# Performance work log

Measured on AMD Instinct MI355X. Metric: run time of the kernel, lower is better.

## Reference

```python
import jax, jax.numpy as jnp
import numpy as np


def _jac_det(u):
    # u: [B, 3, D, H, W] displacement field in [-1, 1]-normalized coords
    B, C, D, H, W = u.shape
    scale = jnp.array([(D - 1) / 2.0, (H - 1) / 2.0, (W - 1) / 2.0], dtype=u.dtype)
    phi = u * scale[None, :, None, None, None]
    px, py, pz = phi[:, 0], phi[:, 1], phi[:, 2]  # each [B, D, H, W]
    # torch.gradient == numpy.gradient: central differences interior, one-sided edges
    gx = lambda a: jnp.gradient(a, axis=-3)
    gy = lambda a: jnp.gradient(a, axis=-2)
    gz = lambda a: jnp.gradient(a, axis=-1)
    dxx = gx(px) + 1.0
    dxy = gy(px)
    dxz = gz(px)
    dyx = gx(py)
    dyy = gy(py) + 1.0
    dyz = gz(py)
    dzx = gx(pz)
    dzy = gy(pz)
    dzz = gz(pz) + 1.0
    det = (dxx * (dyy * dzz - dyz * dzy)
           + dxy * (dyz * dzx - dyx * dzz)
           + dxz * (dyx * dzy - dyy * dzx))
    return det


def setup_inputs() -> dict:
    key = jax.random.key(0)
    displacement_field = jax.random.normal(key, (2, 3, 160, 192, 160), dtype=jnp.float32) * 0.05
    return {"displacement_field": displacement_field}


def reference(displacement_field):
    det = _jac_det(displacement_field)
    # loss = mean(relu(-det))
    return jnp.mean(jax.nn.relu(-det))
```

## Files before the change

kernel.cpp:

```cpp
#include <hip/hip_runtime.h>

#define Dd 160
#define Hh 192
#define Ww 160
#define HW (Hh * Ww)
#define DHW ((size_t)Dd * HW)
#define NVOX_D 9830400.0

#define TH 8
#define TD 10
#define QROW (Ww / 4)
#define TPB (QROW * TH)
#define NHT (Hh / TH)
#define NDS (Dd / TD)
#define GRID1 (2 * NHT * NDS)
#define BLK2 256

__device__ __forceinline__ float4 ld4(const float* p) {
    return *reinterpret_cast<const float4*>(p);
}

__device__ __forceinline__ float4 wgrad(float4 cc, float lft, float rgt, int w0) {
    float4 g;
    g.x = (w0 == 0)      ? (cc.y - cc.x) : 0.5f * (cc.y - lft);
    g.y = 0.5f * (cc.z - cc.x);
    g.z = 0.5f * (cc.w - cc.y);
    g.w = (w0 + 4 == Ww) ? (cc.w - cc.z) : 0.5f * (rgt - cc.z);
    return g;
}

__device__ __forceinline__ float relu_negdet(
    float gd0, float gh0, float gw0,
    float gd1, float gh1, float gw1,
    float gd2, float gh2, float gw2)
{
    const float sx = 79.5f;
    const float sy = 95.5f;
    const float sz = 79.5f;
    float dxx = fmaf(sx, gd0, 1.0f);
    float dxy = sx * gh0;
    float dxz = sx * gw0;
    float dyx = sy * gd1;
    float dyy = fmaf(sy, gh1, 1.0f);
    float dyz = sy * gw1;
    float dzx = sz * gd2;
    float dzy = sz * gh2;
    float dzz = fmaf(sz, gw2, 1.0f);
    float det = dxx * (dyy * dzz - dyz * dzy)
              + dxy * (dyz * dzx - dyx * dzz)
              + dxz * (dyx * dzy - dyy * dzx);
    return fmaxf(-det, 0.0f);
}

__global__ __launch_bounds__(TPB) void jac_partial(const float* __restrict__ u,
                                                   float* __restrict__ part)
{
    const int gid = blockIdx.x;
    const int ds  = gid % NDS;
    const int ht  = (gid / NDS) % NHT;
    const int b   = gid / (NDS * NHT);

    const int tid = threadIdx.x;
    const int wq  = tid % QROW;
    const int hh  = tid / QROW;
    const int h   = ht * TH + hh;
    const int w0  = wq * 4;

    const int hm = (h > 0)      ? h - 1 : 0;
    const int hp = (h < Hh - 1) ? h + 1 : Hh - 1;
    const float hinv = 1.0f / (float)(hp - hm);
    const int offm = (hm - h) * Ww;
    const int offp = (hp - h) * Ww;

    const int d0 = ds * TD;

    const float* pcA = u + (size_t)(b * 3 + 0) * DHW + (size_t)h * Ww + w0;
    const float* pcB = pcA + DHW;
    const float* pcC = pcA + 2 * DHW;

    float4 a0, a1, b0, b1, c0, c1;
    {
        const size_t om = (size_t)((d0 > 0) ? d0 - 1 : 0) * HW;
        const size_t oc = (size_t)d0 * HW;
        a0 = ld4(pcA + om);  a1 = ld4(pcA + oc);
        b0 = ld4(pcB + om);  b1 = ld4(pcB + oc);
        c0 = ld4(pcC + om);  c1 = ld4(pcC + oc);
    }

    float acc = 0.0f;

    #pragma unroll 2
    for (int d = d0; d < d0 + TD; ++d) {
        const int dp = (d < Dd - 1) ? d + 1 : Dd - 1;
        const float dinv = (d > 0 && d < Dd - 1) ? 0.5f : 1.0f;
        const size_t od  = (size_t)d  * HW;
        const size_t odp = (size_t)dp * HW;

        float4 a2 = ld4(pcA + odp);
        float4 b2 = ld4(pcB + odp);
        float4 c2 = ld4(pcC + odp);

        const float* pdA = pcA + od;
        const float* pdB = pcB + od;
        const float* pdC = pcC + od;

        float4 rAm = ld4(pdA + offm), rAp = ld4(pdA + offp);
        float4 rBm = ld4(pdB + offm), rBp = ld4(pdB + offp);
        float4 rCm = ld4(pdC + offm), rCp = ld4(pdC + offp);

        float lA = (w0 > 0) ? pdA[-1] : 0.0f;
        float lB = (w0 > 0) ? pdB[-1] : 0.0f;
        float lC = (w0 > 0) ? pdC[-1] : 0.0f;
        float rA = (w0 + 4 < Ww) ? pdA[4] : 0.0f;
        float rB = (w0 + 4 < Ww) ? pdB[4] : 0.0f;
        float rC = (w0 + 4 < Ww) ? pdC[4] : 0.0f;

        float4 gwA = wgrad(a1, lA, rA, w0);
        float4 gwB = wgrad(b1, lB, rB, w0);
        float4 gwC = wgrad(c1, lC, rC, w0);

        float4 ghA = make_float4((rAp.x - rAm.x) * hinv, (rAp.y - rAm.y) * hinv,
                                 (rAp.z - rAm.z) * hinv, (rAp.w - rAm.w) * hinv);
        float4 ghB = make_float4((rBp.x - rBm.x) * hinv, (rBp.y - rBm.y) * hinv,
                                 (rBp.z - rBm.z) * hinv, (rBp.w - rBm.w) * hinv);
        float4 ghC = make_float4((rCp.x - rCm.x) * hinv, (rCp.y - rCm.y) * hinv,
                                 (rCp.z - rCm.z) * hinv, (rCp.w - rCm.w) * hinv);

        float4 gdA = make_float4((a2.x - a0.x) * dinv, (a2.y - a0.y) * dinv,
                                 (a2.z - a0.z) * dinv, (a2.w - a0.w) * dinv);
        float4 gdB = make_float4((b2.x - b0.x) * dinv, (b2.y - b0.y) * dinv,
                                 (b2.z - b0.z) * dinv, (b2.w - b0.w) * dinv);
        float4 gdC = make_float4((c2.x - c0.x) * dinv, (c2.y - c0.y) * dinv,
                                 (c2.z - c0.z) * dinv, (c2.w - c0.w) * dinv);

        acc += relu_negdet(gdA.x, ghA.x, gwA.x, gdB.x, ghB.x, gwB.x, gdC.x, ghC.x, gwC.x)
             + relu_negdet(gdA.y, ghA.y, gwA.y, gdB.y, ghB.y, gwB.y, gdC.y, ghC.y, gwC.y)
             + relu_negdet(gdA.z, ghA.z, gwA.z, gdB.z, ghB.z, gwB.z, gdC.z, ghC.z, gwC.z)
             + relu_negdet(gdA.w, ghA.w, gwA.w, gdB.w, ghB.w, gwB.w, gdC.w, ghC.w, gwC.w);

        a0 = a1; a1 = a2;
        b0 = b1; b1 = b2;
        c0 = c1; c1 = c2;
    }

    #pragma unroll
    for (int off = 32; off > 0; off >>= 1)
        acc += __shfl_down(acc, off, 64);
    __shared__ float sred[TPB / 64];
    const int lane = tid & 63;
    const int wid  = tid >> 6;
    if (lane == 0) sred[wid] = acc;
    __syncthreads();
    if (tid == 0)
        part[blockIdx.x] = ((sred[0] + sred[1]) + (sred[2] + sred[3])) + sred[4];
}

__global__ __launch_bounds__(BLK2) void jac_final(const float* __restrict__ part,
                                                  float* __restrict__ out)
{
    const int t = threadIdx.x;
    double a = (double)part[t] + (double)part[t + 256] + (double)part[t + 512];
    __shared__ double s[BLK2];
    s[t] = a;
    __syncthreads();
    #pragma unroll
    for (int off = BLK2 / 2; off > 0; off >>= 1) {
        if (t < off) s[t] += s[t + off];
        __syncthreads();
    }
    if (t == 0)
        out[0] = (float)(s[0] / NVOX_D);
}

extern "C" void kernel_launch(void* const* d_in, const int* in_sizes, int n_in,
                              void* d_out, int out_size, void* d_ws, size_t ws_size,
                              hipStream_t stream)
{
    const float* u = (const float*)d_in[0];
    float* part = (float*)d_ws;

    jac_partial<<<GRID1, TPB, 0, stream>>>(u, part);
    jac_final<<<1, BLK2, 0, stream>>>(part, (float*)d_out);
}
```

Baseline: 38.64 us.

## Remap blocks per XCD and alternate depth sweep direction for L2 locality

Block indices are remapped so that contiguous chunks of logical tiles land on the same XCD. This is meant to let neighbouring depth slabs that share halo planes hit the same L2. Odd slabs also sweep depth in reverse, so adjacent slabs start near each other's shared boundary planes at about the same time. Partial sums are written at the logical index, and the reversed sweep flips the sign of the depth-gradient scale to stay correct. This adds a little index arithmetic and assumes the round-robin block-to-XCD dispatch that MI-series GPUs use.

```diff
diff --git a/kernel.cpp b/kernel.cpp
--- a/kernel.cpp
+++ b/kernel.cpp
@@ -14,6 +14,8 @@
 #define NHT (Hh / TH)
 #define NDS (Dd / TD)
 #define GRID1 (2 * NHT * NDS)
+#define NXCD 8
+#define CHUNK (GRID1 / NXCD)
 #define BLK2 256
 
 __device__ __forceinline__ float4 ld4(const float* p) {
@@ -55,10 +57,10 @@
 __global__ __launch_bounds__(TPB) void jac_partial(const float* __restrict__ u,
                                                    float* __restrict__ part)
 {
-    const int gid = blockIdx.x;
-    const int ds  = gid % NDS;
-    const int ht  = (gid / NDS) % NHT;
-    const int b   = gid / (NDS * NHT);
+    const int lg  = (blockIdx.x % NXCD) * CHUNK + blockIdx.x / NXCD;
+    const int ds  = lg % NDS;
+    const int ht  = (lg / NDS) % NHT;
+    const int b   = lg / (NDS * NHT);
 
     const int tid = threadIdx.x;
     const int wq  = tid % QROW;
@@ -72,7 +74,9 @@
     const int offm = (hm - h) * Ww;
     const int offp = (hp - h) * Ww;
 
-    const int d0 = ds * TD;
+    const int d0     = ds * TD;
+    const int dir    = (ds & 1) ? -1 : 1;
+    const int dstart = (dir > 0) ? d0 : d0 + TD - 1;
 
     const float* pcA = u + (size_t)(b * 3 + 0) * DHW + (size_t)h * Ww + w0;
     const float* pcB = pcA + DHW;
@@ -80,8 +84,10 @@
 
     float4 a0, a1, b0, b1, c0, c1;
     {
-        const size_t om = (size_t)((d0 > 0) ? d0 - 1 : 0) * HW;
-        const size_t oc = (size_t)d0 * HW;
+        int db = dstart - dir;
+        db = (db < 0) ? 0 : ((db > Dd - 1) ? Dd - 1 : db);
+        const size_t om = (size_t)db * HW;
+        const size_t oc = (size_t)dstart * HW;
         a0 = ld4(pcA + om);  a1 = ld4(pcA + oc);
         b0 = ld4(pcB + om);  b1 = ld4(pcB + oc);
         c0 = ld4(pcC + om);  c1 = ld4(pcC + oc);
@@ -90,15 +96,17 @@
     float acc = 0.0f;
 
     #pragma unroll 2
-    for (int d = d0; d < d0 + TD; ++d) {
-        const int dp = (d < Dd - 1) ? d + 1 : Dd - 1;
-        const float dinv = (d > 0 && d < Dd - 1) ? 0.5f : 1.0f;
+    for (int i = 0; i < TD; ++i) {
+        const int d  = dstart + dir * i;
+        int dn = d + dir;
+        dn = (dn < 0) ? 0 : ((dn > Dd - 1) ? Dd - 1 : dn);
+        const float dinvs = (float)dir * ((d > 0 && d < Dd - 1) ? 0.5f : 1.0f);
         const size_t od  = (size_t)d  * HW;
-        const size_t odp = (size_t)dp * HW;
+        const size_t odn = (size_t)dn * HW;
 
-        float4 a2 = ld4(pcA + odp);
-        float4 b2 = ld4(pcB + odp);
-        float4 c2 = ld4(pcC + odp);
+        float4 a2 = ld4(pcA + odn);
+        float4 b2 = ld4(pcB + odn);
+        float4 c2 = ld4(pcC + odn);
 
         const float* pdA = pcA + od;
         const float* pdB = pcB + od;
@@ -126,12 +134,12 @@
         float4 ghC = make_float4((rCp.x - rCm.x) * hinv, (rCp.y - rCm.y) * hinv,
                                  (rCp.z - rCm.z) * hinv, (rCp.w - rCm.w) * hinv);
 
-        float4 gdA = make_float4((a2.x - a0.x) * dinv, (a2.y - a0.y) * dinv,
-                                 (a2.z - a0.z) * dinv, (a2.w - a0.w) * dinv);
-        float4 gdB = make_float4((b2.x - b0.x) * dinv, (b2.y - b0.y) * dinv,
-                                 (b2.z - b0.z) * dinv, (b2.w - b0.w) * dinv);
-        float4 gdC = make_float4((c2.x - c0.x) * dinv, (c2.y - c0.y) * dinv,
-                                 (c2.z - c0.z) * dinv, (c2.w - c0.w) * dinv);
+        float4 gdA = make_float4((a2.x - a0.x) * dinvs, (a2.y - a0.y) * dinvs,
+                                 (a2.z - a0.z) * dinvs, (a2.w - a0.w) * dinvs);
+        float4 gdB = make_float4((b2.x - b0.x) * dinvs, (b2.y - b0.y) * dinvs,
+                                 (b2.z - b0.z) * dinvs, (b2.w - b0.w) * dinvs);
+        float4 gdC = make_float4((c2.x - c0.x) * dinvs, (c2.y - c0.y) * dinvs,
+                                 (c2.z - c0.z) * dinvs, (c2.w - c0.w) * dinvs);
 
         acc += relu_negdet(gdA.x, ghA.x, gwA.x, gdB.x, ghB.x, gwB.x, gdC.x, ghC.x, gwC.x)
              + relu_negdet(gdA.y, ghA.y, gwA.y, gdB.y, ghB.y, gwB.y, gdC.y, ghC.y, gwC.y)
@@ -152,7 +160,7 @@
     if (lane == 0) sred[wid] = acc;
     __syncthreads();
     if (tid == 0)
-        part[blockIdx.x] = ((sred[0] + sred[1]) + (sred[2] + sred[3])) + sred[4];
+        part[lg] = ((sred[0] + sred[1]) + (sred[2] + sred[3])) + sred[4];
 }
 
 __global__ __launch_bounds__(BLK2) void jac_final(const float* __restrict__ part,
```

Result: no change. 38.02 us (-1.6%).
